# Performance work log

Hardware: AMD Instinct MI355X
Metric: run time of the kernel (lower is better)

## Reference

```python
import jax, jax.numpy as jnp
import numpy as np

HEADS = 16
DIM_HEAD = 64


def setup_inputs() -> dict:
    key = jax.random.key(0)
    k1, k2, k3, k4 = jax.random.split(key, 4)
    b, sq, skv, dim = 2, 2048, 2048, 1024
    inner = HEADS * DIM_HEAD
    return {
        "x_q": jax.random.normal(k1, (b, sq, dim), dtype=jnp.float32),
        "x_kv": jax.random.normal(k2, (b, skv, dim), dtype=jnp.float32),
        "W_qkv": jax.random.normal(k3, (dim, 3 * inner), dtype=jnp.float32) * (dim ** -0.5),
        "W_out": jax.random.normal(k4, (inner, dim), dtype=jnp.float32) * (inner ** -0.5),
        "b_out": jnp.zeros((dim,), dtype=jnp.float32),
    }


def reference(x_q, x_kv, W_qkv, W_out, b_out):
    b, sq, dim = x_q.shape
    skv = x_kv.shape[1]
    inner = HEADS * DIM_HEAD
    scale = DIM_HEAD ** -0.5
    # to_qkv on concat([x_q, x_kv], seq) as in the original (bias-free linear)
    qkv = jnp.concatenate([x_q, x_kv], axis=1) @ W_qkv  # [b, sq+skv, 3*inner]
    q, k, v = jnp.split(qkv, 3, axis=-1)
    q = q[:, :sq].reshape(b, sq, HEADS, DIM_HEAD).transpose(0, 2, 1, 3)   # [b,h,sq,d]
    k = k[:, sq:].reshape(b, skv, HEADS, DIM_HEAD).transpose(0, 2, 1, 3)  # [b,h,skv,d]
    v = v[:, sq:].reshape(b, skv, HEADS, DIM_HEAD).transpose(0, 2, 1, 3)  # [b,h,skv,d]
    dots = jnp.einsum('bhqd,bhkd->bhqk', q, k) * scale
    attn = jax.nn.softmax(dots, axis=-1)  # dropout p=0.0 -> identity
    out = jnp.einsum('bhqk,bhkd->bhqd', attn, v)
    out = out.transpose(0, 2, 1, 3).reshape(b, sq, inner)
    return out @ W_out + b_out
```

## Files before the change

### kernel.cpp

```cpp
#include <hip/hip_runtime.h>


typedef __attribute__((ext_vector_type(8))) short short8;
typedef __attribute__((ext_vector_type(4))) short short4v;
typedef __attribute__((ext_vector_type(4))) float floatx4;

#define QSCALE 0.18033688f

#if __has_builtin(__builtin_amdgcn_exp2f)
#define EXP2(x) __builtin_amdgcn_exp2f(x)
#else
#define EXP2(x) exp2f(x)
#endif

__device__ __forceinline__ ushort f2b(float f) {
  union { float f; unsigned u; } x; x.f = f;
  unsigned r = (x.u + 0x7fffu + ((x.u >> 16) & 1u)) >> 16;
  return (ushort)r;
}

__device__ __forceinline__ unsigned f2b2(float a, float b) {
  union { float f; unsigned u; } x, y; x.f = a; y.f = b;
  return __builtin_amdgcn_perm(y.u + 0x8000u, x.u + 0x8000u, 0x07060302u);
}

#define GLL(gp, lp)                                                            \
  __builtin_amdgcn_global_load_lds(                                            \
      (const __attribute__((address_space(1))) void*)(gp),                     \
      (__attribute__((address_space(3))) void*)(lp), 16, 0, 0)

__global__ void prep(const float* __restrict__ xq, const float* __restrict__ xkv,
                     ushort* __restrict__ oq, ushort* __restrict__ okv,
                     const float* __restrict__ Wqkv, ushort* __restrict__ WqkvT,
                     const float* __restrict__ Wout, ushort* __restrict__ WoutT) {
  __shared__ float tile[32][33];
  int bid = blockIdx.x;
  const int n = 4096 * 1024;
  if (bid < 2048) {
    bool lo = bid < 1024;
    const float* in = lo ? xq : xkv;
    ushort* out = lo ? oq : okv;
    int b2 = lo ? bid : bid - 1024;
    int stride = 1024 * 256 * 4;
    for (int i = (b2 * 256 + (int)threadIdx.x) * 4; i < n; i += stride) {
      float4 v = *(const float4*)(in + i);
      uint2 o;
      o.x = f2b2(v.x, v.y);
      o.y = f2b2(v.z, v.w);
      *(uint2*)(out + i) = o;
    }
    return;
  }
  int tb = bid - 2048;
  int bx = tb & 127, by = tb >> 7;
  bool first = bx < 96;
  const float* in = first ? Wqkv : Wout;
  ushort* out = first ? WqkvT : WoutT;
  int N = first ? 3072 : 1024;
  int bxx = first ? bx : bx - 96;
  int k0 = by * 32, n0 = bxx * 32;
  int tx = threadIdx.x & 31, ty = threadIdx.x >> 5;
#pragma unroll
  for (int i = 0; i < 32; i += 8)
    tile[ty + i][tx] = in[(size_t)(k0 + ty + i) * N + n0 + tx];
  __syncthreads();
#pragma unroll
  for (int i = 0; i < 32; i += 8)
    out[(size_t)(n0 + ty + i) * 1024 + k0 + tx] = f2b(tile[tx][ty + i]);
}

__global__ __launch_bounds__(256, 3) void gemm_qkv(
    const ushort* __restrict__ Aq, const ushort* __restrict__ Akv,
    const ushort* __restrict__ Bt,
    ushort* __restrict__ Cq, ushort* __restrict__ Ck, ushort* __restrict__ Cv) {
  __shared__ __align__(16) ushort smem[17408];
  ushort* Asb = smem;
  ushort* Bsb = smem + 8192;
  const int n0 = blockIdx.x * 128, m0 = blockIdx.y * 128;
  const ushort* A = (blockIdx.x >= 8) ? Akv : Aq;
  const int t = threadIdx.x;
  const int w = t >> 6, lane = t & 63, dl = lane & 15, g = lane >> 4;
  const int wm = (w >> 1) * 64, wn = (w & 1) * 64;
  const int K = 1024;

  auto stage = [&](int buf, int k0) {
#pragma unroll
    for (int p = 0; p < 2; p++) {
      int j = t + p * 256;
      int row = j >> 2, slot = j & 3, c = (slot - row) & 3;
      GLL(A + (size_t)(m0 + row) * K + k0 + c * 8, &Asb[buf * 4096 + j * 8]);
    }
#pragma unroll
    for (int p = 0; p < 2; p++) {
      int j = t + p * 256;
      int row = j >> 2, slot = j & 3, c = (slot - row) & 3;
      GLL(Bt + (size_t)(n0 + row) * K + k0 + c * 8, &Bsb[buf * 4096 + j * 8]);
    }
  };

  const floatx4 fz = {0.f, 0.f, 0.f, 0.f};
  floatx4 acc[4][4];
#pragma unroll
  for (int i = 0; i < 4; i++)
#pragma unroll
    for (int j = 0; j < 4; j++) acc[i][j] = fz;

  stage(0, 0);
  for (int kt = 0; kt < 32; kt++) {
    int cur = kt & 1;
    __builtin_amdgcn_s_waitcnt(0);
    __syncthreads();
    if (kt + 1 < 32) stage(cur ^ 1, (kt + 1) * 32);
    short8 af[4], bf[4];
#pragma unroll
    for (int mt = 0; mt < 4; mt++) {
      int row = wm + mt * 16 + dl;
      af[mt] = *(const short8*)&Asb[cur * 4096 + row * 32 + ((g + row) & 3) * 8];
    }
#pragma unroll
    for (int nt = 0; nt < 4; nt++) {
      int row = wn + nt * 16 + dl;
      bf[nt] = *(const short8*)&Bsb[cur * 4096 + row * 32 + ((g + row) & 3) * 8];
    }
#pragma unroll
    for (int mt = 0; mt < 4; mt++)
#pragma unroll
      for (int nt = 0; nt < 4; nt++)
        acc[mt][nt] = __builtin_amdgcn_mfma_f32_16x16x32_bf16(af[mt], bf[nt], acc[mt][nt], 0, 0, 0);
  }

  if (blockIdx.x < 16) {
#pragma unroll
    for (int mt = 0; mt < 4; mt++)
#pragma unroll
      for (int nt = 0; nt < 4; nt++) {
        int gcol = n0 + wn + nt * 16 + dl;
        int row0 = m0 + wm + mt * 16 + g * 4;
        if (gcol < 1024) {
#pragma unroll
          for (int r = 0; r < 4; r++)
            Cq[(size_t)(row0 + r) * 1024 + gcol] = f2b(acc[mt][nt][r] * QSCALE);
        } else {
#pragma unroll
          for (int r = 0; r < 4; r++)
            Ck[(size_t)(row0 + r) * 1024 + gcol - 1024] = f2b(acc[mt][nt][r]);
        }
      }
  } else {
    __syncthreads();
#pragma unroll
    for (int mt = 0; mt < 4; mt++)
#pragma unroll
      for (int nt = 0; nt < 4; nt++) {
        int ncol = wn + nt * 16 + dl;
        int mrow = wm + mt * 16 + g * 4;
        uint2 pk;
        pk.x = f2b2(acc[mt][nt][0], acc[mt][nt][1]);
        pk.y = f2b2(acc[mt][nt][2], acc[mt][nt][3]);
        *(uint2*)&smem[ncol * 136 + mrow] = pk;
      }
    __syncthreads();
    int hd0 = n0 - 2048;
    int bb = m0 >> 11;
    int kv0 = m0 & 2047;
#pragma unroll
    for (int p = 0; p < 8; p++) {
      int j = t + p * 256;
      int row = j >> 4, c = j & 15;
      short8 v = *(const short8*)&smem[row * 136 + c * 8];
      *(short8*)(Cv + ((size_t)(bb * 1024 + hd0 + row)) * 2048 + kv0 + c * 8) = v;
    }
  }
}

__global__ __launch_bounds__(256, 3) void gemm_out(
    const ushort* __restrict__ A, const ushort* __restrict__ Bt,
    float* __restrict__ C, const float* __restrict__ bias) {
  __shared__ __align__(16) ushort As[2][128 * 64];
  __shared__ __align__(16) ushort Bs[2][64 * 64];
  const int n0 = blockIdx.x * 64, m0 = blockIdx.y * 128;
  const int t = threadIdx.x;
  const int w = t >> 6, lane = t & 63, dl = lane & 15, g = lane >> 4;
  const int wm = (w >> 1) * 64, wn = (w & 1) * 32;
  const int K = 1024;

  auto stage = [&](int buf, int k0) {
#pragma unroll
    for (int p = 0; p < 4; p++) {
      int j = t + p * 256;
      int row = j >> 3, slot = j & 7, c = (slot - row) & 7;
      GLL(A + (size_t)(m0 + row) * K + k0 + c * 8, &As[buf][j * 8]);
    }
#pragma unroll
    for (int p = 0; p < 2; p++) {
      int j = t + p * 256;
      int row = j >> 3, slot = j & 7, c = (slot - row) & 7;
      GLL(Bt + (size_t)(n0 + row) * K + k0 + c * 8, &Bs[buf][j * 8]);
    }
  };

  const floatx4 fz = {0.f, 0.f, 0.f, 0.f};
  floatx4 acc[4][2];
#pragma unroll
  for (int i = 0; i < 4; i++)
#pragma unroll
    for (int j = 0; j < 2; j++) acc[i][j] = fz;

  stage(0, 0);
  for (int kt = 0; kt < 16; kt++) {
    int cur = kt & 1;
    __builtin_amdgcn_s_waitcnt(0);
    __syncthreads();
    if (kt + 1 < 16) stage(cur ^ 1, (kt + 1) * 64);
#pragma unroll
    for (int ks = 0; ks < 2; ks++) {
      short8 af[4], bf[2];
#pragma unroll
      for (int mt = 0; mt < 4; mt++) {
        int row = wm + mt * 16 + dl;
        af[mt] = *(const short8*)&As[cur][row * 64 + ((ks * 4 + g + row) & 7) * 8];
      }
#pragma unroll
      for (int nt = 0; nt < 2; nt++) {
        int row = wn + nt * 16 + dl;
        bf[nt] = *(const short8*)&Bs[cur][row * 64 + ((ks * 4 + g + row) & 7) * 8];
      }
#pragma unroll
      for (int mt = 0; mt < 4; mt++)
#pragma unroll
        for (int nt = 0; nt < 2; nt++)
          acc[mt][nt] = __builtin_amdgcn_mfma_f32_16x16x32_bf16(af[mt], bf[nt], acc[mt][nt], 0, 0, 0);
    }
  }
#pragma unroll
  for (int mt = 0; mt < 4; mt++)
#pragma unroll
    for (int nt = 0; nt < 2; nt++) {
      int gcol = n0 + wn + nt * 16 + dl;
      int row0 = m0 + wm + mt * 16 + g * 4;
      float badd = bias[gcol];
#pragma unroll
      for (int r = 0; r < 4; r++)
        C[(size_t)(row0 + r) * 1024 + gcol] = acc[mt][nt][r] + badd;
    }
}

__global__ __launch_bounds__(256, 2) void attn(
    const ushort* __restrict__ Qb,
    const ushort* __restrict__ Kb,
    const ushort* __restrict__ Vt,
    ushort* __restrict__ Ob) {
  __shared__ __align__(16) ushort Ks[2][64 * 64];
  __shared__ __align__(16) ushort Vs[2][64 * 64];
  __shared__ __align__(16) ushort Pq[128 * 64];

  const int bh = blockIdx.x, b = bh >> 4, h = bh & 15;
  const int q0 = blockIdx.y * 128;
  const int t = threadIdx.x, w = t >> 6, lane = t & 63, dl = lane & 15, g = lane >> 4;

  const ushort* Kg = Kb + (size_t)(b * 2048) * 1024 + h * 64;
  const ushort* Vg = Vt + (size_t)(b * 1024 + h * 64) * 2048;

  short8 bq[2][2];
#pragma unroll
  for (int nt = 0; nt < 2; nt++) {
    int qa = q0 + w * 32 + nt * 16 + dl;
    const ushort* qrow = Qb + (size_t)(b * 2048 + qa) * 1024 + h * 64;
    bq[nt][0] = *(const short8*)(qrow + g * 8);
    bq[nt][1] = *(const short8*)(qrow + 32 + g * 8);
  }

  auto stageK = [&](int buf, int kv0) {
#pragma unroll
    for (int p = 0; p < 2; p++) {
      int j = t + p * 256;
      int row = j >> 3, slot = j & 7, c = (slot - row) & 7;
      GLL(Kg + (size_t)(kv0 + row) * 1024 + c * 8, &Ks[buf][j * 8]);
    }
  };
  auto stageV = [&](int buf, int kv0) {
#pragma unroll
    for (int p = 0; p < 2; p++) {
      int j = t + p * 256;
      int row = j >> 3, slot = j & 7, c = (slot - row) & 7;
      GLL(Vg + (size_t)row * 2048 + kv0 + c * 8, &Vs[buf][j * 8]);
    }
  };
  stageK(0, 0);
  stageV(0, 0);

  const floatx4 fz = {0.f, 0.f, 0.f, 0.f};
  floatx4 o[4][2];
#pragma unroll
  for (int i = 0; i < 4; i++)
#pragma unroll
    for (int n = 0; n < 2; n++) o[i][n] = fz;
  floatx4 l4[2] = {fz, fz};

  for (int it = 0; it < 32; it++) {
    int cur = it & 1;
    __builtin_amdgcn_s_waitcnt(0);
    __syncthreads();
    if (it + 1 < 32) { stageK(cur ^ 1, (it + 1) * 64); stageV(cur ^ 1, (it + 1) * 64); }

    floatx4 s[4][2];
#pragma unroll
    for (int mt = 0; mt < 4; mt++)
#pragma unroll
      for (int nt = 0; nt < 2; nt++) s[mt][nt] = fz;
#pragma unroll
    for (int ks = 0; ks < 2; ks++) {
      short8 a[4];
#pragma unroll
      for (int mt = 0; mt < 4; mt++) {
        int row = mt * 16 + dl;
        a[mt] = *(const short8*)&Ks[cur][row * 64 + ((ks * 4 + g + row) & 7) * 8];
      }
#pragma unroll
      for (int mt = 0; mt < 4; mt++)
#pragma unroll
        for (int nt = 0; nt < 2; nt++)
          s[mt][nt] = __builtin_amdgcn_mfma_f32_16x16x32_bf16(a[mt], bq[nt][ks], s[mt][nt], 0, 0, 0);
    }

#pragma unroll
    for (int nt = 0; nt < 2; nt++)
#pragma unroll
      for (int mt = 0; mt < 4; mt++) {
#pragma unroll
        for (int r = 0; r < 4; r++) s[mt][nt][r] = EXP2(s[mt][nt][r]);
        l4[nt] += s[mt][nt];
      }

#pragma unroll
    for (int nt = 0; nt < 2; nt++) {
      int qr = w * 32 + nt * 16 + dl;
#pragma unroll
      for (int mt = 0; mt < 4; mt++) {
        uint2 pk;
        pk.x = f2b2(s[mt][nt][0], s[mt][nt][1]);
        pk.y = f2b2(s[mt][nt][2], s[mt][nt][3]);
        *(uint2*)&Pq[qr * 64 + ((mt * 4 + g + qr) & 15) * 4] = pk;
      }
    }
    asm volatile("" ::: "memory");

#pragma unroll
    for (int ks2 = 0; ks2 < 2; ks2++) {
      short8 av[4], bp[2];
#pragma unroll
      for (int mtd = 0; mtd < 4; mtd++) {
        int row = mtd * 16 + dl;
        av[mtd] = *(const short8*)&Vs[cur][row * 64 + ((ks2 * 4 + g + row) & 7) * 8];
      }
#pragma unroll
      for (int nt = 0; nt < 2; nt++) {
        int qr = w * 32 + nt * 16 + dl;
        int sq = ks2 * 8 + 2 * g;
        short4v lo = *(const short4v*)&Pq[qr * 64 + ((sq + qr) & 15) * 4];
        short4v hi = *(const short4v*)&Pq[qr * 64 + ((sq + 1 + qr) & 15) * 4];
        bp[nt] = short8{lo.x, lo.y, lo.z, lo.w, hi.x, hi.y, hi.z, hi.w};
      }
#pragma unroll
      for (int mtd = 0; mtd < 4; mtd++)
#pragma unroll
        for (int nt = 0; nt < 2; nt++)
          o[mtd][nt] = __builtin_amdgcn_mfma_f32_16x16x32_bf16(av[mtd], bp[nt], o[mtd][nt], 0, 0, 0);
    }
    asm volatile("" ::: "memory");
  }

  float inv_l[2];
#pragma unroll
  for (int nt = 0; nt < 2; nt++) {
    float l = (l4[nt][0] + l4[nt][1]) + (l4[nt][2] + l4[nt][3]);
    l += __shfl_xor(l, 16);
    l += __shfl_xor(l, 32);
    inv_l[nt] = 1.f / l;
  }

#pragma unroll
  for (int nt = 0; nt < 2; nt++) {
    int qr = w * 32 + nt * 16 + dl;
#pragma unroll
    for (int mtd = 0; mtd < 4; mtd++) {
      uint2 pk;
      pk.x = f2b2(o[mtd][nt][0] * inv_l[nt], o[mtd][nt][1] * inv_l[nt]);
      pk.y = f2b2(o[mtd][nt][2] * inv_l[nt], o[mtd][nt][3] * inv_l[nt]);
      *(uint2*)&Pq[qr * 64 + ((mtd * 4 + g + qr) & 15) * 4] = pk;
    }
  }
  asm volatile("" ::: "memory");
#pragma unroll
  for (int p = 0; p < 4; p++) {
    int j = lane + p * 64;
    int r32 = j >> 3, c = j & 7;
    int qr = w * 32 + r32;
    short4v lo = *(const short4v*)&Pq[qr * 64 + ((2 * c + qr) & 15) * 4];
    short4v hi = *(const short4v*)&Pq[qr * 64 + ((2 * c + 1 + qr) & 15) * 4];
    short8 v = {lo.x, lo.y, lo.z, lo.w, hi.x, hi.y, hi.z, hi.w};
    *(short8*)(Ob + (size_t)(b * 2048 + q0 + qr) * 1024 + h * 64 + c * 8) = v;
  }
}

extern "C" void kernel_launch(void* const* d_in, const int* in_sizes, int n_in,
                              void* d_out, int out_size, void* d_ws, size_t ws_size,
                              hipStream_t stream) {
  const float* x_q  = (const float*)d_in[0];
  const float* x_kv = (const float*)d_in[1];
  const float* Wqkv = (const float*)d_in[2];
  const float* Wout = (const float*)d_in[3];
  const float* bout = (const float*)d_in[4];
  float* out = (float*)d_out;

  char* p = (char*)d_ws;
  ushort* Xq    = (ushort*)p; p += (size_t)4096 * 1024 * 2;
  ushort* Xkv   = (ushort*)p; p += (size_t)4096 * 1024 * 2;
  ushort* WqkvT = (ushort*)p; p += (size_t)3072 * 1024 * 2;
  ushort* WoutT = (ushort*)p; p += (size_t)1024 * 1024 * 2;
  ushort* Qb    = (ushort*)p; p += (size_t)4096 * 1024 * 2;
  ushort* Kb    = (ushort*)p; p += (size_t)4096 * 1024 * 2;
  ushort* Vt    = (ushort*)p; p += (size_t)2 * 1024 * 2048 * 2;
  ushort* Ob    = (ushort*)p; p += (size_t)4096 * 1024 * 2;

  prep<<<6144, 256, 0, stream>>>(x_q, x_kv, Xq, Xkv, Wqkv, WqkvT, Wout, WoutT);
  gemm_qkv<<<dim3(24, 32), 256, 0, stream>>>(Xq, Xkv, WqkvT, Qb, Kb, Vt);
  attn<<<dim3(32, 16), 256, 0, stream>>>(Qb, Kb, Vt, Ob);
  gemm_out<<<dim3(16, 32), 256, 0, stream>>>(Ob, WoutT, out, bout);
}
```

Baseline: 195.3 us.

## Switch attention to 32x32x16 MFMA and keep P in registers via permlane swaps

The attention kernel moves from 16x16x32 to 32x32x16 bf16 MFMA tiles for both QK^T and PV. The softmax probabilities are packed with v_cvt_pk_bf16_f32 and redistributed with v_permlane32_swap instead of a round trip through the Pq shared buffer. This removes that LDS buffer and its stores and loads, and the output epilogue now reuses the K buffer. The trade-offs are the lane-layout assumptions of the 32x32 MFMA output, the gfx950-specific instructions, and an extra barrier before the epilogue.

Result: no change. 191.8 us (-1.8%).

```diff
diff --git a/kernel.cpp b/kernel.cpp
--- a/kernel.cpp
+++ b/kernel.cpp
@@ -4,6 +4,7 @@
 typedef __attribute__((ext_vector_type(8))) short short8;
 typedef __attribute__((ext_vector_type(4))) short short4v;
 typedef __attribute__((ext_vector_type(4))) float floatx4;
+typedef __attribute__((ext_vector_type(16))) float floatx16;
 
 #define QSCALE 0.18033688f
 
@@ -22,6 +23,12 @@
 __device__ __forceinline__ unsigned f2b2(float a, float b) {
   union { float f; unsigned u; } x, y; x.f = a; y.f = b;
   return __builtin_amdgcn_perm(y.u + 0x8000u, x.u + 0x8000u, 0x07060302u);
+}
+
+__device__ __forceinline__ unsigned cvtpk(float a, float b) {
+  unsigned r;
+  asm("v_cvt_pk_bf16_f32 %0, %1, %2" : "=v"(r) : "v"(a), "v"(b));
+  return r;
 }
 
 #define GLL(gp, lp)                                                            \
@@ -252,22 +259,22 @@
     ushort* __restrict__ Ob) {
   __shared__ __align__(16) ushort Ks[2][64 * 64];
   __shared__ __align__(16) ushort Vs[2][64 * 64];
-  __shared__ __align__(16) ushort Pq[128 * 64];
 
   const int bh = blockIdx.x, b = bh >> 4, h = bh & 15;
   const int q0 = blockIdx.y * 128;
-  const int t = threadIdx.x, w = t >> 6, lane = t & 63, dl = lane & 15, g = lane >> 4;
+  const int t = threadIdx.x, w = t >> 6, lane = t & 63;
+  const int l31 = lane & 31, l5 = lane >> 5;
 
   const ushort* Kg = Kb + (size_t)(b * 2048) * 1024 + h * 64;
   const ushort* Vg = Vt + (size_t)(b * 1024 + h * 64) * 2048;
 
-  short8 bq[2][2];
-#pragma unroll
-  for (int nt = 0; nt < 2; nt++) {
-    int qa = q0 + w * 32 + nt * 16 + dl;
+  short8 bq[4];
+  {
+    int qa = q0 + w * 32 + l31;
     const ushort* qrow = Qb + (size_t)(b * 2048 + qa) * 1024 + h * 64;
-    bq[nt][0] = *(const short8*)(qrow + g * 8);
-    bq[nt][1] = *(const short8*)(qrow + 32 + g * 8);
+#pragma unroll
+    for (int ks = 0; ks < 4; ks++)
+      bq[ks] = *(const short8*)(qrow + ks * 16 + l5 * 8);
   }
 
   auto stageK = [&](int buf, int kv0) {
@@ -289,13 +296,12 @@
   stageK(0, 0);
   stageV(0, 0);
 
-  const floatx4 fz = {0.f, 0.f, 0.f, 0.f};
-  floatx4 o[4][2];
-#pragma unroll
-  for (int i = 0; i < 4; i++)
-#pragma unroll
-    for (int n = 0; n < 2; n++) o[i][n] = fz;
-  floatx4 l4[2] = {fz, fz};
+  floatx16 o2[2];
+#pragma unroll
+  for (int m2 = 0; m2 < 2; m2++)
+#pragma unroll
+    for (int r = 0; r < 16; r++) o2[m2][r] = 0.f;
+  floatx4 l4 = {0.f, 0.f, 0.f, 0.f};
 
   for (int it = 0; it < 32; it++) {
     int cur = it & 1;
@@ -303,92 +309,74 @@
     __syncthreads();
     if (it + 1 < 32) { stageK(cur ^ 1, (it + 1) * 64); stageV(cur ^ 1, (it + 1) * 64); }
 
-    floatx4 s[4][2];
-#pragma unroll
-    for (int mt = 0; mt < 4; mt++)
-#pragma unroll
-      for (int nt = 0; nt < 2; nt++) s[mt][nt] = fz;
-#pragma unroll
-    for (int ks = 0; ks < 2; ks++) {
-      short8 a[4];
-#pragma unroll
-      for (int mt = 0; mt < 4; mt++) {
-        int row = mt * 16 + dl;
-        a[mt] = *(const short8*)&Ks[cur][row * 64 + ((ks * 4 + g + row) & 7) * 8];
-      }
-#pragma unroll
-      for (int mt = 0; mt < 4; mt++)
-#pragma unroll
-        for (int nt = 0; nt < 2; nt++)
-          s[mt][nt] = __builtin_amdgcn_mfma_f32_16x16x32_bf16(a[mt], bq[nt][ks], s[mt][nt], 0, 0, 0);
-    }
-
-#pragma unroll
-    for (int nt = 0; nt < 2; nt++)
-#pragma unroll
-      for (int mt = 0; mt < 4; mt++) {
-#pragma unroll
-        for (int r = 0; r < 4; r++) s[mt][nt][r] = EXP2(s[mt][nt][r]);
-        l4[nt] += s[mt][nt];
-      }
-
-#pragma unroll
-    for (int nt = 0; nt < 2; nt++) {
-      int qr = w * 32 + nt * 16 + dl;
-#pragma unroll
-      for (int mt = 0; mt < 4; mt++) {
-        uint2 pk;
-        pk.x = f2b2(s[mt][nt][0], s[mt][nt][1]);
-        pk.y = f2b2(s[mt][nt][2], s[mt][nt][3]);
-        *(uint2*)&Pq[qr * 64 + ((mt * 4 + g + qr) & 15) * 4] = pk;
-      }
-    }
-    asm volatile("" ::: "memory");
-
-#pragma unroll
-    for (int ks2 = 0; ks2 < 2; ks2++) {
-      short8 av[4], bp[2];
-#pragma unroll
-      for (int mtd = 0; mtd < 4; mtd++) {
-        int row = mtd * 16 + dl;
-        av[mtd] = *(const short8*)&Vs[cur][row * 64 + ((ks2 * 4 + g + row) & 7) * 8];
-      }
-#pragma unroll
-      for (int nt = 0; nt < 2; nt++) {
-        int qr = w * 32 + nt * 16 + dl;
-        int sq = ks2 * 8 + 2 * g;
-        short4v lo = *(const short4v*)&Pq[qr * 64 + ((sq + qr) & 15) * 4];
-        short4v hi = *(const short4v*)&Pq[qr * 64 + ((sq + 1 + qr) & 15) * 4];
-        bp[nt] = short8{lo.x, lo.y, lo.z, lo.w, hi.x, hi.y, hi.z, hi.w};
-      }
-#pragma unroll
-      for (int mtd = 0; mtd < 4; mtd++)
-#pragma unroll
-        for (int nt = 0; nt < 2; nt++)
-          o[mtd][nt] = __builtin_amdgcn_mfma_f32_16x16x32_bf16(av[mtd], bp[nt], o[mtd][nt], 0, 0, 0);
-    }
-    asm volatile("" ::: "memory");
-  }
-
-  float inv_l[2];
-#pragma unroll
-  for (int nt = 0; nt < 2; nt++) {
-    float l = (l4[nt][0] + l4[nt][1]) + (l4[nt][2] + l4[nt][3]);
-    l += __shfl_xor(l, 16);
-    l += __shfl_xor(l, 32);
-    inv_l[nt] = 1.f / l;
-  }
-
-#pragma unroll
-  for (int nt = 0; nt < 2; nt++) {
-    int qr = w * 32 + nt * 16 + dl;
-#pragma unroll
-    for (int mtd = 0; mtd < 4; mtd++) {
-      uint2 pk;
-      pk.x = f2b2(o[mtd][nt][0] * inv_l[nt], o[mtd][nt][1] * inv_l[nt]);
-      pk.y = f2b2(o[mtd][nt][2] * inv_l[nt], o[mtd][nt][3] * inv_l[nt]);
-      *(uint2*)&Pq[qr * 64 + ((mtd * 4 + g + qr) & 15) * 4] = pk;
-    }
+    floatx16 s2[2];
+#pragma unroll
+    for (int m2 = 0; m2 < 2; m2++)
+#pragma unroll
+      for (int r = 0; r < 16; r++) s2[m2][r] = 0.f;
+#pragma unroll
+    for (int ks = 0; ks < 4; ks++)
+#pragma unroll
+      for (int m2 = 0; m2 < 2; m2++) {
+        int row = m2 * 32 + l31;
+        short8 a = *(const short8*)&Ks[cur][row * 64 + ((ks * 2 + l5 + row) & 7) * 8];
+        s2[m2] = __builtin_amdgcn_mfma_f32_32x32x16_bf16(a, bq[ks], s2[m2], 0, 0, 0);
+      }
+
+#pragma unroll
+    for (int m2 = 0; m2 < 2; m2++)
+#pragma unroll
+      for (int r = 0; r < 16; r++) s2[m2][r] = EXP2(s2[m2][r]);
+#pragma unroll
+    for (int r = 0; r < 16; r++) l4[r & 3] += s2[0][r] + s2[1][r];
+
+    short8 bp[4];
+#pragma unroll
+    for (int m2 = 0; m2 < 2; m2++) {
+      unsigned pk[8];
+#pragma unroll
+      for (int p = 0; p < 8; p++)
+        pk[p] = cvtpk(s2[m2][2 * p], s2[m2][2 * p + 1]);
+#pragma unroll
+      for (int hf = 0; hf < 2; hf++) {
+        unsigned x0 = pk[hf * 4 + 0], y0 = pk[hf * 4 + 2];
+        unsigned x1 = pk[hf * 4 + 1], y1 = pk[hf * 4 + 3];
+        asm("v_permlane32_swap_b32 %0, %1" : "+v"(x0), "+v"(y0));
+        asm("v_permlane32_swap_b32 %0, %1" : "+v"(x1), "+v"(y1));
+        union { unsigned u[4]; short8 s8; } fu;
+        fu.u[0] = x0; fu.u[1] = x1; fu.u[2] = y0; fu.u[3] = y1;
+        bp[m2 * 2 + hf] = fu.s8;
+      }
+    }
+
+#pragma unroll
+    for (int kt = 0; kt < 4; kt++)
+#pragma unroll
+      for (int m2 = 0; m2 < 2; m2++) {
+        int row = m2 * 32 + l31;
+        short8 av = *(const short8*)&Vs[cur][row * 64 + ((kt * 2 + l5 + row) & 7) * 8];
+        o2[m2] = __builtin_amdgcn_mfma_f32_32x32x16_bf16(av, bp[kt], o2[m2], 0, 0, 0);
+      }
+  }
+
+  float l = (l4[0] + l4[1]) + (l4[2] + l4[3]);
+  l += __shfl_xor(l, 32);
+  float inv_l = 1.f / l;
+
+  __syncthreads();
+  ushort* Ot = &Ks[0][0];
+  {
+    int q = w * 32 + l31;
+#pragma unroll
+    for (int m2 = 0; m2 < 2; m2++)
+#pragma unroll
+      for (int pp = 0; pp < 4; pp++) {
+        uint2 pk2;
+        pk2.x = cvtpk(o2[m2][4 * pp + 0] * inv_l, o2[m2][4 * pp + 1] * inv_l);
+        pk2.y = cvtpk(o2[m2][4 * pp + 2] * inv_l, o2[m2][4 * pp + 3] * inv_l);
+        int s = m2 * 8 + 2 * pp + l5;
+        *(uint2*)&Ot[q * 64 + ((s + q) & 15) * 4] = pk2;
+      }
   }
   asm volatile("" ::: "memory");
 #pragma unroll
@@ -396,8 +384,8 @@
     int j = lane + p * 64;
     int r32 = j >> 3, c = j & 7;
     int qr = w * 32 + r32;
-    short4v lo = *(const short4v*)&Pq[qr * 64 + ((2 * c + qr) & 15) * 4];
-    short4v hi = *(const short4v*)&Pq[qr * 64 + ((2 * c + 1 + qr) & 15) * 4];
+    short4v lo = *(const short4v*)&Ot[qr * 64 + ((2 * c + qr) & 15) * 4];
+    short4v hi = *(const short4v*)&Ot[qr * 64 + ((2 * c + 1 + qr) & 15) * 4];
     short8 v = {lo.x, lo.y, lo.z, lo.w, hi.x, hi.y, hi.z, hi.w};
     *(short8*)(Ob + (size_t)(b * 2048 + q0 + qr) * 1024 + h * 64 + c * 8) = v;
   }
```
